# Kernel tuning notes

Measured on AMD Instinct MI355X. Metric: run time of the kernel, lower is better.

## Reference

```python
import jax, jax.numpy as jnp
import numpy as np

D_MODEL = 2048
N_Q_HEADS = 32
N_KV_HEADS = 8
D_HEAD = 64
D_MLP = 8192
NORM_EPS = 1e-5
INIT_RANGE = 0.02
IGNORE = -100000.0
B, S = 2, 2048


def setup_inputs() -> dict:
    key = jax.random.key(0)
    ks = jax.random.split(key, 8)
    return {
        "resid_pre": jax.random.normal(ks[0], (B, S, D_MODEL), dtype=jnp.float32),
        "W_Q": jax.random.normal(ks[1], (N_Q_HEADS, D_MODEL, D_HEAD), dtype=jnp.float32) * INIT_RANGE,
        "W_K": jax.random.normal(ks[2], (N_KV_HEADS, D_MODEL, D_HEAD), dtype=jnp.float32) * INIT_RANGE,
        "W_V": jax.random.normal(ks[3], (N_KV_HEADS, D_MODEL, D_HEAD), dtype=jnp.float32) * INIT_RANGE,
        "W_O": jax.random.normal(ks[4], (N_KV_HEADS, D_HEAD, D_MODEL), dtype=jnp.float32) * INIT_RANGE,
        "g1": jnp.ones((D_MODEL,), jnp.float32),
        "b1": jnp.zeros((D_MODEL,), jnp.float32),
        "g2": jnp.ones((D_MODEL,), jnp.float32),
        "b2": jnp.zeros((D_MODEL,), jnp.float32),
        "W_in": jax.random.normal(ks[5], (D_MODEL, D_MLP), dtype=jnp.float32) * INIT_RANGE,
        "b_in": jnp.zeros((D_MLP,), jnp.float32),
        "W_out": jax.random.normal(ks[6], (D_MLP, D_MODEL), dtype=jnp.float32) * INIT_RANGE,
        "b_out": jnp.zeros((D_MODEL,), jnp.float32),
    }


def rmsnorm(x, g, b):
    # torch.var (unbiased=False) is mean-centered variance, but x itself is
    # divided (not centered) -- faithful to the source.
    mu = jnp.mean(x, axis=-1, keepdims=True)
    var = jnp.mean(jnp.square(x - mu), axis=-1, keepdims=True)
    std = jnp.sqrt(var + NORM_EPS)
    return (x / std) * g + b


def attention(x, W_Q, W_K, W_V, W_O):
    b, s, _ = x.shape
    q = jnp.einsum('bpd,hde->bphe', x, W_Q)            # [b, s, n_q, d_head]
    k = jnp.einsum('bpd,hde->bphe', x, W_K)            # [b, s, n_kv, d_head]
    v = jnp.einsum('bpd,hde->bphe', x, W_V)            # [b, s, n_kv, d_head]
    g_size = N_Q_HEADS // N_KV_HEADS
    # rearrange '(n_kv g) d' with n_kv outer, group inner
    q = q.reshape(b, s, N_KV_HEADS, g_size, D_HEAD)
    # source einsum sums over the group dim (g not in output) -- faithful
    scores = jnp.einsum('bqkgd,bskd->bkqs', q, k) / jnp.sqrt(jnp.float32(D_HEAD))
    mask = jnp.triu(jnp.ones((s, s), dtype=bool), k=1)
    scores = jnp.where(mask, jnp.float32(IGNORE), scores)
    pattern = jax.nn.softmax(scores, axis=-1)          # [b, n_kv, q, s]
    z = jnp.einsum('bskd,bkqs->bqkd', v, pattern)      # [b, q, n_kv, d_head]
    return jnp.einsum('bqkd,kde->bqe', z, W_O)


def ffn(x, W_in, b_in, W_out, b_out):
    pre = jnp.einsum('bpd,dm->bpm', x, W_in) + b_in
    post = jax.nn.relu(pre)
    return jnp.einsum('bpm,md->bpd', post, W_out) + b_out


def reference(resid_pre, W_Q, W_K, W_V, W_O, g1, b1, g2, b2, W_in, b_in, W_out, b_out):
    resid_mid = attention(rmsnorm(resid_pre, g1, b1), W_Q, W_K, W_V, W_O) + resid_pre
    resid_post = ffn(rmsnorm(resid_mid, g2, b2), W_in, b_in, W_out, b_out) + resid_mid
    return resid_post
```

## Files before the change

kernel.cpp:

```cpp
#include <hip/hip_runtime.h>
#include <hip/hip_bf16.h>


using bf16 = __hip_bfloat16;
typedef __bf16 bf16x8_t __attribute__((ext_vector_type(8)));
typedef float  f32x4_t  __attribute__((ext_vector_type(4)));

#define D_MODEL 2048
#define SEQ     2048
#define NB      2
#define NTOK    4096
#define NKV     8
#define DHEAD   64
#define DMLP    8192
#define NQKV    1536

__device__ inline void storev(float* p, float v) { *p = v; }
__device__ inline void storev(bf16* p, float v)  { *p = __float2bfloat16(v); }

__device__ inline __bf16 tobf(float x) {
    union { __hip_bfloat16 h; __bf16 b; } u;
    u.h = __float2bfloat16(x);
    return u.b;
}

__global__ __launch_bounds__(256) void transpose_f32_bf16_kernel(
    const float* __restrict__ in, bf16* __restrict__ out, int K, int N)
{
    __shared__ float tile[32][33];
    const int n0 = blockIdx.x * 32, k0 = blockIdx.y * 32;
    const int tx = threadIdx.x & 31, ty = threadIdx.x >> 5;
    #pragma unroll
    for (int i = 0; i < 32; i += 8)
        tile[ty + i][tx] = in[(size_t)(k0 + ty + i) * N + n0 + tx];
    __syncthreads();
    #pragma unroll
    for (int i = 0; i < 32; i += 8)
        out[(size_t)(n0 + ty + i) * K + k0 + tx] = __float2bfloat16(tile[tx][ty + i]);
}

__global__ __launch_bounds__(256) void head_transpose_kernel(
    const float* __restrict__ in, bf16* __restrict__ out, int ngroup)
{
    __shared__ float tile[32][65];
    const int kv = blockIdx.y;
    const int k0 = blockIdx.x * 32;
    const int t  = threadIdx.x;
    const int e  = t & 63, kk = t >> 6;
    #pragma unroll
    for (int i = 0; i < 32; i += 4) {
        float s = 0.f;
        for (int g = 0; g < ngroup; ++g)
            s += in[((size_t)(kv * ngroup + g) * 2048 + k0 + kk + i) * 64 + e];
        tile[kk + i][e] = s;
    }
    __syncthreads();
    const int k = t & 31, ee = t >> 5;
    #pragma unroll
    for (int i = 0; i < 64; i += 8)
        out[(size_t)(kv * 64 + ee + i) * 2048 + k0 + k] = __float2bfloat16(tile[k][ee + i]);
}

__global__ __launch_bounds__(256) void rmsnorm_kernel(
    const float* __restrict__ x, const float* __restrict__ g,
    const float* __restrict__ b, bf16* __restrict__ out)
{
    const int row = blockIdx.x;
    const int t = threadIdx.x;
    const float* xr = x + (size_t)row * D_MODEL;
    float4 a0 = *reinterpret_cast<const float4*>(xr + t * 8);
    float4 a1 = *reinterpret_cast<const float4*>(xr + t * 8 + 4);
    float v[8] = {a0.x, a0.y, a0.z, a0.w, a1.x, a1.y, a1.z, a1.w};
    float sum = 0.f, sumsq = 0.f;
    #pragma unroll
    for (int j = 0; j < 8; ++j) { sum += v[j]; sumsq += v[j] * v[j]; }
    #pragma unroll
    for (int o = 1; o < 64; o <<= 1) {
        sum   += __shfl_xor(sum, o);
        sumsq += __shfl_xor(sumsq, o);
    }
    __shared__ float rs[4], rq[4];
    if ((t & 63) == 0) { rs[t >> 6] = sum; rq[t >> 6] = sumsq; }
    __syncthreads();
    sum   = rs[0] + rs[1] + rs[2] + rs[3];
    sumsq = rq[0] + rq[1] + rq[2] + rq[3];
    const float mu  = sum * (1.f / D_MODEL);
    const float var = sumsq * (1.f / D_MODEL) - mu * mu;
    const float rstd = 1.f / sqrtf(var + 1e-5f);
    const int c = t * 8;
    float4 g0 = *reinterpret_cast<const float4*>(g + c);
    float4 g1 = *reinterpret_cast<const float4*>(g + c + 4);
    float4 b0 = *reinterpret_cast<const float4*>(b + c);
    float4 b1 = *reinterpret_cast<const float4*>(b + c + 4);
    float gg[8] = {g0.x, g0.y, g0.z, g0.w, g1.x, g1.y, g1.z, g1.w};
    float bb[8] = {b0.x, b0.y, b0.z, b0.w, b1.x, b1.y, b1.z, b1.w};
    bf16* op = out + (size_t)row * D_MODEL + c;
    #pragma unroll
    for (int j = 0; j < 8; ++j) op[j] = __float2bfloat16(v[j] * rstd * gg[j] + bb[j]);
}

template<int BM, int BN, typename TC, bool BIAS, bool RELU, bool RESID>
__global__ __launch_bounds__(512, 2) void gemm_pipe_kernel(
    const bf16* __restrict__ A, const bf16* __restrict__ Bt,
    TC* __restrict__ C, const float* __restrict__ bias,
    const float* __restrict__ resid, int M, int N, int K, int nbx)
{
    constexpr int BK   = 64;
    constexpr int MREP = BM / 32;
    constexpr int NREP = BN / 64;
    constexpr int AI   = (BM * BK) / 4096;
    constexpr int BI   = (BN * BK) / 4096;
    constexpr int LD   = AI + BI;

    __shared__ __align__(16) bf16 As[2][BM * BK];
    __shared__ __align__(16) bf16 Bs[2][BN * BK];

    const int nwg = gridDim.x;
    const int swz = (blockIdx.x & 7) * (nwg >> 3) + (blockIdx.x >> 3);
    const int nby = nwg / nbx;
    const int by  = swz % nby;
    const int bx  = swz / nby;
    const int row0 = by * BM, col0 = bx * BN;

    const int t  = threadIdx.x;
    const int w  = t >> 6, ln = t & 63;
    const int wm = w >> 2, wn = w & 3;
    const int lr = ln & 15, hi = ln >> 4;

    const int srow = w * 8 + (ln >> 3);
    const int skx  = ((ln & 7) ^ (ln >> 3)) * 8;

    f32x4_t acc[MREP][NREP];
    #pragma unroll
    for (int m = 0; m < MREP; ++m)
        #pragma unroll
        for (int n = 0; n < NREP; ++n) acc[m][n] = (f32x4_t){0.f, 0.f, 0.f, 0.f};

    const int NT = K / BK;

    {
        const bf16* ga = A  + (size_t)(row0 + srow) * K + skx;
        const bf16* gb = Bt + (size_t)(col0 + srow) * K + skx;
        #pragma unroll
        for (int i = 0; i < AI; ++i)
            __builtin_amdgcn_global_load_lds(
                (const __attribute__((address_space(1))) void*)(ga + (size_t)i * 64 * K),
                (__attribute__((address_space(3))) void*)(&As[0][i * 4096 + w * 512]), 16, 0, 0);
        #pragma unroll
        for (int i = 0; i < BI; ++i)
            __builtin_amdgcn_global_load_lds(
                (const __attribute__((address_space(1))) void*)(gb + (size_t)i * 64 * K),
                (__attribute__((address_space(3))) void*)(&Bs[0][i * 4096 + w * 512]), 16, 0, 0);
    }

    for (int tt = 0; tt < NT; ++tt) {
        const int c = tt & 1;
        asm volatile("s_waitcnt lgkmcnt(0)" ::: "memory");
        __builtin_amdgcn_sched_barrier(0);
        __builtin_amdgcn_s_barrier();
        __builtin_amdgcn_sched_barrier(0);
        if (tt + 1 < NT) {
            const int d = c ^ 1;
            const int kt = (tt + 1) * BK;
            const bf16* ga = A  + (size_t)(row0 + srow) * K + kt + skx;
            const bf16* gb = Bt + (size_t)(col0 + srow) * K + kt + skx;
            #pragma unroll
            for (int i = 0; i < AI; ++i)
                __builtin_amdgcn_global_load_lds(
                    (const __attribute__((address_space(1))) void*)(ga + (size_t)i * 64 * K),
                    (__attribute__((address_space(3))) void*)(&As[d][i * 4096 + w * 512]), 16, 0, 0);
            #pragma unroll
            for (int i = 0; i < BI; ++i)
                __builtin_amdgcn_global_load_lds(
                    (const __attribute__((address_space(1))) void*)(gb + (size_t)i * 64 * K),
                    (__attribute__((address_space(3))) void*)(&Bs[d][i * 4096 + w * 512]), 16, 0, 0);
            __builtin_amdgcn_sched_barrier(0);
            if constexpr (LD == 8)      asm volatile("s_waitcnt vmcnt(8)" ::: "memory");
            else if constexpr (LD == 6) asm volatile("s_waitcnt vmcnt(6)" ::: "memory");
            else                        asm volatile("s_waitcnt vmcnt(4)" ::: "memory");
        } else {
            asm volatile("s_waitcnt vmcnt(0)" ::: "memory");
        }
        __builtin_amdgcn_sched_barrier(0);
        __builtin_amdgcn_s_barrier();
        __builtin_amdgcn_sched_barrier(0);

        #pragma unroll
        for (int kk = 0; kk < 2; ++kk) {
            bf16x8_t af[MREP], bfr[NREP];
            #pragma unroll
            for (int m = 0; m < MREP; ++m) {
                const int row = wm * (BM / 2) + m * 16 + lr;
                af[m] = *reinterpret_cast<const bf16x8_t*>(
                    &As[c][row * 64 + ((kk * 32 + hi * 8) ^ ((row & 7) << 3))]);
            }
            #pragma unroll
            for (int n = 0; n < NREP; ++n) {
                const int col = wn * (BN / 4) + n * 16 + lr;
                bfr[n] = *reinterpret_cast<const bf16x8_t*>(
                    &Bs[c][col * 64 + ((kk * 32 + hi * 8) ^ ((col & 7) << 3))]);
            }
            #pragma unroll
            for (int m = 0; m < MREP; ++m)
                #pragma unroll
                for (int n = 0; n < NREP; ++n)
                    acc[m][n] = __builtin_amdgcn_mfma_f32_16x16x32_bf16(af[m], bfr[n], acc[m][n], 0, 0, 0);
        }
    }

    #pragma unroll
    for (int m = 0; m < MREP; ++m) {
        #pragma unroll
        for (int n = 0; n < NREP; ++n) {
            const int cgl = col0 + wn * (BN / 4) + n * 16 + lr;
            #pragma unroll
            for (int j = 0; j < 4; ++j) {
                const int r = row0 + wm * (BM / 2) + m * 16 + hi * 4 + j;
                float v = acc[m][n][j];
                if constexpr (BIAS)  v += bias[cgl];
                if constexpr (RELU)  v = fmaxf(v, 0.f);
                if constexpr (RESID) v += resid[(size_t)r * N + cgl];
                storev(&C[(size_t)r * N + cgl], v);
            }
        }
    }
}

template<int BN, typename TC, bool BIAS, bool RELU, bool RESID>
__global__ __launch_bounds__(512, 2) void gemm_8ph_kernel(
    const bf16* __restrict__ A, const bf16* __restrict__ Bt,
    TC* __restrict__ C, const float* __restrict__ bias,
    const float* __restrict__ resid, int M, int N, int K, int nbx)
{
    constexpr int NREP = BN / 64;
    constexpr int NH   = NREP / 2;
    constexpr int BI   = BN / 64;

    __shared__ __align__(16) bf16 As[2][256 * 64];
    __shared__ __align__(16) bf16 Bs[2][BN * 64];

    const int nwg = gridDim.x;
    const int swz = (blockIdx.x & 7) * (nwg >> 3) + (blockIdx.x >> 3);
    const int nby = nwg / nbx;
    const int by  = swz % nby;
    const int bx  = swz / nby;
    const int row0 = by * 256, col0 = bx * BN;

    const int t  = threadIdx.x;
    const int w  = t >> 6, ln = t & 63;
    const int wm = w >> 2, wn = w & 3;
    const int lr = ln & 15, hi = ln >> 4;
    const int rx = (lr & 7) << 3;

    const int srow = w * 8 + (ln >> 3);
    const int skx  = ((ln & 7) ^ (ln >> 3)) * 8;

#define STAGE_A8(u, dbuf, kt)                                                   \
    __builtin_amdgcn_global_load_lds(                                           \
        (const __attribute__((address_space(1))) void*)(A + (size_t)(row0 + (u) * 64 + srow) * K + (kt) + skx), \
        (__attribute__((address_space(3))) void*)(&As[dbuf][(u) * 4096 + w * 512]), 16, 0, 0)
#define STAGE_B8(u, dbuf, kt)                                                   \
    __builtin_amdgcn_global_load_lds(                                           \
        (const __attribute__((address_space(1))) void*)(Bt + (size_t)(col0 + (u) * 64 + srow) * K + (kt) + skx), \
        (__attribute__((address_space(3))) void*)(&Bs[dbuf][(u) * 4096 + w * 512]), 16, 0, 0)
#define PH_BAR                                                                  \
    __builtin_amdgcn_sched_barrier(0);                                          \
    __builtin_amdgcn_s_barrier();                                               \
    __builtin_amdgcn_sched_barrier(0)
#define LGKM0                                                                   \
    asm volatile("s_waitcnt lgkmcnt(0)" ::: "memory");                          \
    __builtin_amdgcn_sched_barrier(0)

    f32x4_t acc[8][NREP];
    #pragma unroll
    for (int m = 0; m < 8; ++m)
        #pragma unroll
        for (int n = 0; n < NREP; ++n) acc[m][n] = (f32x4_t){0.f, 0.f, 0.f, 0.f};

    bf16x8_t af[4][2];
    bf16x8_t bfr[NREP][2];

    const int NT = K / 64;

    STAGE_A8(0, 0, 0); STAGE_A8(2, 0, 0);
    #pragma unroll
    for (int u = 0; u < BI; ++u) STAGE_B8(u, 0, 0);
    STAGE_A8(1, 0, 0); STAGE_A8(3, 0, 0);
    asm volatile("s_waitcnt vmcnt(2)" ::: "memory");
    PH_BAR;

    for (int tt = 0; tt < NT; ++tt) {
        const int c  = tt & 1, d = c ^ 1;
        const int kn = (tt + 1) * 64;
        const bool pf = (tt + 1 < NT);

        #pragma unroll
        for (int mq = 0; mq < 4; ++mq) {
            const int row = wm * 128 + mq * 16 + lr;
            #pragma unroll
            for (int kk = 0; kk < 2; ++kk)
                af[mq][kk] = *reinterpret_cast<const bf16x8_t*>(
                    &As[c][row * 64 + ((kk * 32 + hi * 8) ^ rx)]);
        }
        #pragma unroll
        for (int n = 0; n < NH; ++n) {
            const int col = wn * (BN / 4) + n * 16 + lr;
            #pragma unroll
            for (int kk = 0; kk < 2; ++kk)
                bfr[n][kk] = *reinterpret_cast<const bf16x8_t*>(
                    &Bs[c][col * 64 + ((kk * 32 + hi * 8) ^ rx)]);
        }
        if (pf) { STAGE_A8(0, d, kn); STAGE_A8(2, d, kn); }
        PH_BAR;
        LGKM0;
        __builtin_amdgcn_s_setprio(1);
        #pragma unroll
        for (int mq = 0; mq < 4; ++mq)
            #pragma unroll
            for (int n = 0; n < NH; ++n)
                #pragma unroll
                for (int kk = 0; kk < 2; ++kk)
                    acc[mq][n] = __builtin_amdgcn_mfma_f32_16x16x32_bf16(af[mq][kk], bfr[n][kk], acc[mq][n], 0, 0, 0);
        __builtin_amdgcn_s_setprio(0);
        PH_BAR;

        #pragma unroll
        for (int n = NH; n < NREP; ++n) {
            const int col = wn * (BN / 4) + n * 16 + lr;
            #pragma unroll
            for (int kk = 0; kk < 2; ++kk)
                bfr[n][kk] = *reinterpret_cast<const bf16x8_t*>(
                    &Bs[c][col * 64 + ((kk * 32 + hi * 8) ^ rx)]);
        }
        if (pf) { STAGE_B8(0, d, kn); STAGE_B8(1, d, kn); }
        __builtin_amdgcn_sched_barrier(0);
        if (pf) { asm volatile("s_waitcnt vmcnt(4)" ::: "memory"); }
        else    { asm volatile("s_waitcnt vmcnt(0)" ::: "memory"); }
        PH_BAR;
        LGKM0;
        __builtin_amdgcn_s_setprio(1);
        #pragma unroll
        for (int mq = 0; mq < 4; ++mq)
            #pragma unroll
            for (int n = NH; n < NREP; ++n)
                #pragma unroll
                for (int kk = 0; kk < 2; ++kk)
                    acc[mq][n] = __builtin_amdgcn_mfma_f32_16x16x32_bf16(af[mq][kk], bfr[n][kk], acc[mq][n], 0, 0, 0);
        __builtin_amdgcn_s_setprio(0);
        PH_BAR;

        #pragma unroll
        for (int mq = 0; mq < 4; ++mq) {
            const int row = wm * 128 + 64 + mq * 16 + lr;
            #pragma unroll
            for (int kk = 0; kk < 2; ++kk)
                af[mq][kk] = *reinterpret_cast<const bf16x8_t*>(
                    &As[c][row * 64 + ((kk * 32 + hi * 8) ^ rx)]);
        }
        if (pf) { if constexpr (BI == 4) { STAGE_B8(2, d, kn); STAGE_B8(3, d, kn); } }
        PH_BAR;
        LGKM0;
        __builtin_amdgcn_s_setprio(1);
        #pragma unroll
        for (int mq = 0; mq < 4; ++mq)
            #pragma unroll
            for (int n = NH; n < NREP; ++n)
                #pragma unroll
                for (int kk = 0; kk < 2; ++kk)
                    acc[4 + mq][n] = __builtin_amdgcn_mfma_f32_16x16x32_bf16(af[mq][kk], bfr[n][kk], acc[4 + mq][n], 0, 0, 0);
        __builtin_amdgcn_s_setprio(0);
        PH_BAR;

        if (pf) {
            STAGE_A8(1, d, kn); STAGE_A8(3, d, kn);
            __builtin_amdgcn_sched_barrier(0);
            asm volatile("s_waitcnt vmcnt(2)" ::: "memory");
        }
        PH_BAR;
        __builtin_amdgcn_s_setprio(1);
        #pragma unroll
        for (int mq = 0; mq < 4; ++mq)
            #pragma unroll
            for (int n = 0; n < NH; ++n)
                #pragma unroll
                for (int kk = 0; kk < 2; ++kk)
                    acc[4 + mq][n] = __builtin_amdgcn_mfma_f32_16x16x32_bf16(af[mq][kk], bfr[n][kk], acc[4 + mq][n], 0, 0, 0);
        __builtin_amdgcn_s_setprio(0);
        PH_BAR;
    }

    #pragma unroll
    for (int m = 0; m < 8; ++m) {
        #pragma unroll
        for (int n = 0; n < NREP; ++n) {
            const int cgl = col0 + wn * (BN / 4) + n * 16 + lr;
            #pragma unroll
            for (int j = 0; j < 4; ++j) {
                const int r = row0 + wm * 128 + m * 16 + hi * 4 + j;
                float v = acc[m][n][j];
                if constexpr (BIAS)  v += bias[cgl];
                if constexpr (RELU)  v = fmaxf(v, 0.f);
                if constexpr (RESID) v += resid[(size_t)r * N + cgl];
                storev(&C[(size_t)r * N + cgl], v);
            }
        }
    }
#undef STAGE_A8
#undef STAGE_B8
#undef PH_BAR
#undef LGKM0
}

#define KVBLK 64
#define LP    72

__global__ __launch_bounds__(256) void mfma_attn_kernel(
    const float* __restrict__ qkv, bf16* __restrict__ z)
{
    const int a  = blockIdx.x;
    const int kv = blockIdx.y;
    const int b  = blockIdx.z;
    const int b2 = 31 - a;
    const int t  = threadIdx.x;
    const int w  = t >> 6;
    const int ln = t & 63;
    const int lr = ln & 15;
    const int hi = ln >> 4;
    const int lk = hi * 8;

    __shared__ __align__(16) bf16 Ks[KVBLK * LP];
    __shared__ __align__(16) bf16 Vt[DHEAD * LP];
    __shared__ __align__(16) bf16 Ps[64 * LP];

    bf16x8_t qfA[2], qfB[2];
    #pragma unroll
    for (int sb = 0; sb < 2; ++sb) {
        const int qrow = (sb ? b2 : a) * 64 + w * 16 + lr;
        const float* qp = qkv + (size_t)(b * SEQ + qrow) * NQKV + kv * 64;
        #pragma unroll
        for (int kk = 0; kk < 2; ++kk) {
            float4 x0 = *reinterpret_cast<const float4*>(qp + kk * 32 + lk);
            float4 x1 = *reinterpret_cast<const float4*>(qp + kk * 32 + lk + 4);
            bf16x8_t v;
            v[0] = tobf(x0.x); v[1] = tobf(x0.y); v[2] = tobf(x0.z); v[3] = tobf(x0.w);
            v[4] = tobf(x1.x); v[5] = tobf(x1.y); v[6] = tobf(x1.z); v[7] = tobf(x1.w);
            if (sb) qfB[kk] = v; else qfA[kk] = v;
        }
    }

    f32x4_t accA[4], accB[4];
    #pragma unroll
    for (int n = 0; n < 4; ++n) {
        accA[n] = (f32x4_t){0.f, 0.f, 0.f, 0.f};
        accB[n] = (f32x4_t){0.f, 0.f, 0.f, 0.f};
    }
    float mA[4] = {-1e30f, -1e30f, -1e30f, -1e30f}, lA[4] = {0.f, 0.f, 0.f, 0.f};
    float mB[4] = {-1e30f, -1e30f, -1e30f, -1e30f}, lB[4] = {0.f, 0.f, 0.f, 0.f};

    const int qcdA = a  * 64 + w * 16 + hi * 4;
    const int qcdB = b2 * 64 + w * 16 + hi * 4;

    auto process = [&](const bf16x8_t* qf, f32x4_t* acc_o, float* m_st,
                       float* l_st, int qcd, int k0g, bool diag) {
        f32x4_t s[4];
        #pragma unroll
        for (int n = 0; n < 4; ++n) s[n] = (f32x4_t){0.f, 0.f, 0.f, 0.f};
        #pragma unroll
        for (int kk = 0; kk < 2; ++kk) {
            #pragma unroll
            for (int n = 0; n < 4; ++n) {
                bf16x8_t kf = *reinterpret_cast<const bf16x8_t*>(&Ks[(n * 16 + lr) * LP + kk * 32 + lk]);
                s[n] = __builtin_amdgcn_mfma_f32_16x16x32_bf16(qf[kk], kf, s[n], 0, 0, 0);
            }
        }
        #pragma unroll
        for (int n = 0; n < 4; ++n) {
            const int colg = k0g + n * 16 + lr;
            #pragma unroll
            for (int j = 0; j < 4; ++j) {
                float val = s[n][j] * 0.125f;
                if (diag && colg > qcd + j) val = -1e30f;
                s[n][j] = val;
            }
        }
        float alpha[4], mnew[4];
        #pragma unroll
        for (int j = 0; j < 4; ++j) {
            float mx = fmaxf(fmaxf(s[0][j], s[1][j]), fmaxf(s[2][j], s[3][j]));
            mx = fmaxf(mx, __shfl_xor(mx, 1));
            mx = fmaxf(mx, __shfl_xor(mx, 2));
            mx = fmaxf(mx, __shfl_xor(mx, 4));
            mx = fmaxf(mx, __shfl_xor(mx, 8));
            mnew[j]  = fmaxf(m_st[j], mx);
            alpha[j] = __expf(m_st[j] - mnew[j]);
            m_st[j]  = mnew[j];
        }
        float psum[4] = {0.f, 0.f, 0.f, 0.f};
        #pragma unroll
        for (int n = 0; n < 4; ++n) {
            #pragma unroll
            for (int j = 0; j < 4; ++j) {
                float p = __expf(s[n][j] - mnew[j]);
                psum[j] += p;
                Ps[(w * 16 + hi * 4 + j) * LP + n * 16 + lr] = __float2bfloat16(p);
            }
        }
        #pragma unroll
        for (int j = 0; j < 4; ++j) {
            float ps = psum[j];
            ps += __shfl_xor(ps, 1);
            ps += __shfl_xor(ps, 2);
            ps += __shfl_xor(ps, 4);
            ps += __shfl_xor(ps, 8);
            l_st[j] = l_st[j] * alpha[j] + ps;
        }
        #pragma unroll
        for (int n = 0; n < 4; ++n)
            #pragma unroll
            for (int j = 0; j < 4; ++j)
                acc_o[n][j] *= alpha[j];
        #pragma unroll
        for (int kk = 0; kk < 2; ++kk) {
            bf16x8_t pa = *reinterpret_cast<const bf16x8_t*>(&Ps[(w * 16 + lr) * LP + kk * 32 + lk]);
            #pragma unroll
            for (int n = 0; n < 4; ++n) {
                bf16x8_t vf = *reinterpret_cast<const bf16x8_t*>(&Vt[(n * 16 + lr) * LP + kk * 32 + lk]);
                acc_o[n] = __builtin_amdgcn_mfma_f32_16x16x32_bf16(pa, vf, acc_o[n], 0, 0, 0);
            }
        }
    };

    for (int kt = 0; kt <= b2; ++kt) {
        const int k0g = kt * KVBLK;
        __syncthreads();
        {
            const int r   = t >> 2;
            const int c16 = (t & 3) * 16;
            const float* kb = qkv + (size_t)(b * SEQ + k0g + r) * NQKV + 512 + kv * 64 + c16;
            #pragma unroll
            for (int h = 0; h < 2; ++h) {
                float4 k0 = *reinterpret_cast<const float4*>(kb + h * 8);
                float4 k1 = *reinterpret_cast<const float4*>(kb + h * 8 + 4);
                bf16x8_t kvv;
                kvv[0] = tobf(k0.x); kvv[1] = tobf(k0.y); kvv[2] = tobf(k0.z); kvv[3] = tobf(k0.w);
                kvv[4] = tobf(k1.x); kvv[5] = tobf(k1.y); kvv[6] = tobf(k1.z); kvv[7] = tobf(k1.w);
                *reinterpret_cast<bf16x8_t*>(&Ks[r * LP + c16 + h * 8]) = kvv;
            }
        }
        {
            const int dv = w * 16;
            const float* vb = qkv + (size_t)(b * SEQ + k0g + ln) * NQKV + 1024 + kv * 64 + dv;
            #pragma unroll
            for (int h = 0; h < 4; ++h) {
                float4 v4 = *reinterpret_cast<const float4*>(vb + h * 4);
                Vt[(dv + h * 4 + 0) * LP + ln] = __float2bfloat16(v4.x);
                Vt[(dv + h * 4 + 1) * LP + ln] = __float2bfloat16(v4.y);
                Vt[(dv + h * 4 + 2) * LP + ln] = __float2bfloat16(v4.z);
                Vt[(dv + h * 4 + 3) * LP + ln] = __float2bfloat16(v4.w);
            }
        }
        __syncthreads();

        if (kt <= a) process(qfA, accA, mA, lA, qcdA, k0g, kt == a);
        process(qfB, accB, mB, lB, qcdB, k0g, kt == b2);
    }

    #pragma unroll
    for (int j = 0; j < 4; ++j) {
        const float invA = 1.f / lA[j];
        bf16* zpA = z + (size_t)(b * SEQ + qcdA + j) * (NKV * DHEAD) + kv * 64;
        const float invB = 1.f / lB[j];
        bf16* zpB = z + (size_t)(b * SEQ + qcdB + j) * (NKV * DHEAD) + kv * 64;
        #pragma unroll
        for (int n = 0; n < 4; ++n) {
            zpA[n * 16 + lr] = __float2bfloat16(accA[n][j] * invA);
            zpB[n * 16 + lr] = __float2bfloat16(accB[n][j] * invB);
        }
    }
}

extern "C" void kernel_launch(void* const* d_in, const int* in_sizes, int n_in,
                              void* d_out, int out_size, void* d_ws, size_t ws_size,
                              hipStream_t stream)
{
    const float* resid_pre = (const float*)d_in[0];
    const float* W_Q   = (const float*)d_in[1];
    const float* W_K   = (const float*)d_in[2];
    const float* W_V   = (const float*)d_in[3];
    const float* W_O   = (const float*)d_in[4];
    const float* g1    = (const float*)d_in[5];
    const float* b1    = (const float*)d_in[6];
    const float* g2    = (const float*)d_in[7];
    const float* b2    = (const float*)d_in[8];
    const float* W_in  = (const float*)d_in[9];
    const float* b_in  = (const float*)d_in[10];
    const float* W_out = (const float*)d_in[11];
    const float* b_out = (const float*)d_in[12];
    float* out = (float*)d_out;

    char* ws = (char*)d_ws;
    const size_t OFF_WBIG  = 0;
    const size_t OFF_WOT   = OFF_WBIG + (size_t)DMLP * D_MODEL * 2;
    const size_t OFF_X1    = OFF_WOT  + (size_t)D_MODEL * 512 * 2;
    const size_t OFF_RMID  = OFF_X1   + (size_t)NTOK * D_MODEL * 2;
    const size_t OFF_POST  = OFF_RMID + (size_t)NTOK * D_MODEL * 4;
    const size_t OFF_WQKVT = OFF_POST;
    const size_t OFF_QKV   = OFF_WQKVT + (size_t)NQKV * D_MODEL * 2;
    const size_t OFF_Z     = OFF_QKV   + (size_t)NTOK * NQKV * 4;

    bf16*  winT   = (bf16*) (ws + OFF_WBIG);
    bf16*  woutT  = (bf16*) (ws + OFF_WBIG);
    bf16*  woT    = (bf16*) (ws + OFF_WOT);
    bf16*  x1     = (bf16*) (ws + OFF_X1);
    float* rmid   = (float*)(ws + OFF_RMID);
    bf16*  post   = (bf16*) (ws + OFF_POST);
    bf16*  wqkvT  = (bf16*) (ws + OFF_WQKVT);
    float* qkv    = (float*)(ws + OFF_QKV);
    bf16*  zbuf   = (bf16*) (ws + OFF_Z);

    transpose_f32_bf16_kernel<<<dim3(DMLP / 32, D_MODEL / 32), 256, 0, stream>>>(W_in, winT, D_MODEL, DMLP);
    head_transpose_kernel<<<dim3(D_MODEL / 32, NKV), 256, 0, stream>>>(W_Q, wqkvT, 4);
    head_transpose_kernel<<<dim3(D_MODEL / 32, NKV), 256, 0, stream>>>(W_K, wqkvT + (size_t)512  * D_MODEL, 1);
    head_transpose_kernel<<<dim3(D_MODEL / 32, NKV), 256, 0, stream>>>(W_V, wqkvT + (size_t)1024 * D_MODEL, 1);
    transpose_f32_bf16_kernel<<<dim3(D_MODEL / 32, 512 / 32), 256, 0, stream>>>(W_O, woT, 512, D_MODEL);

    rmsnorm_kernel<<<NTOK, 256, 0, stream>>>(resid_pre, g1, b1, x1);
    gemm_pipe_kernel<128, 128, float, false, false, false><<<384, 512, 0, stream>>>(
        x1, wqkvT, qkv, nullptr, nullptr, NTOK, NQKV, D_MODEL, NQKV / 128);
    mfma_attn_kernel<<<dim3(16, NKV, NB), 256, 0, stream>>>(qkv, zbuf);
    gemm_pipe_kernel<128, 128, float, false, false, true><<<512, 512, 0, stream>>>(
        zbuf, woT, rmid, nullptr, resid_pre, NTOK, D_MODEL, 512, D_MODEL / 128);
    rmsnorm_kernel<<<NTOK, 256, 0, stream>>>(rmid, g2, b2, x1);
    gemm_8ph_kernel<256, bf16, true, true, false><<<512, 512, 0, stream>>>(
        x1, winT, post, b_in, nullptr, NTOK, DMLP, D_MODEL, DMLP / 256);
    transpose_f32_bf16_kernel<<<dim3(D_MODEL / 32, DMLP / 32), 256, 0, stream>>>(W_out, woutT, DMLP, D_MODEL);
    gemm_8ph_kernel<128, float, true, false, true><<<256, 512, 0, stream>>>(
        post, woutT, out, b_out, rmid, NTOK, D_MODEL, DMLP, D_MODEL / 128);
}
```

Before: 535.5 us.

## Store QKV in bf16 and switch the W_out GEMM to 128x128 tiles

The QKV projection now writes bf16 instead of fp32. The attention kernel loads Q, K and V directly as bf16 vectors, which halves the QKV traffic and removes the per-element conversions. The final FFN down-projection moves from the 256x128 8-phase kernel with 256 blocks to the 128x128 pipelined kernel with 512 blocks, giving more blocks for the 256 CUs. The 8-phase kernel is specialized to BN=256, and the qcdB indexing is rewritten as an explicit formula.

```diff
diff --git a/kernel.cpp b/kernel.cpp
--- a/kernel.cpp
+++ b/kernel.cpp
@@ -18,10 +18,10 @@
 __device__ inline void storev(float* p, float v) { *p = v; }
 __device__ inline void storev(bf16* p, float v)  { *p = __float2bfloat16(v); }
 
-__device__ inline __bf16 tobf(float x) {
-    union { __hip_bfloat16 h; __bf16 b; } u;
-    u.h = __float2bfloat16(x);
-    return u.b;
+__device__ inline bf16 h_from_b(__bf16 x) {
+    union { __bf16 b; bf16 h; } u;
+    u.b = x;
+    return u.h;
 }
 
 __global__ __launch_bounds__(256) void transpose_f32_bf16_kernel(
@@ -226,25 +226,21 @@
     }
 }
 
-template<int BN, typename TC, bool BIAS, bool RELU, bool RESID>
+template<typename TC, bool BIAS, bool RELU, bool RESID>
 __global__ __launch_bounds__(512, 2) void gemm_8ph_kernel(
     const bf16* __restrict__ A, const bf16* __restrict__ Bt,
     TC* __restrict__ C, const float* __restrict__ bias,
     const float* __restrict__ resid, int M, int N, int K, int nbx)
 {
-    constexpr int NREP = BN / 64;
-    constexpr int NH   = NREP / 2;
-    constexpr int BI   = BN / 64;
-
     __shared__ __align__(16) bf16 As[2][256 * 64];
-    __shared__ __align__(16) bf16 Bs[2][BN * 64];
+    __shared__ __align__(16) bf16 Bs[2][256 * 64];
 
     const int nwg = gridDim.x;
     const int swz = (blockIdx.x & 7) * (nwg >> 3) + (blockIdx.x >> 3);
     const int nby = nwg / nbx;
     const int by  = swz % nby;
     const int bx  = swz / nby;
-    const int row0 = by * 256, col0 = bx * BN;
+    const int row0 = by * 256, col0 = bx * 256;
 
     const int t  = threadIdx.x;
     const int w  = t >> 6, ln = t & 63;
@@ -271,20 +267,19 @@
     asm volatile("s_waitcnt lgkmcnt(0)" ::: "memory");                          \
     __builtin_amdgcn_sched_barrier(0)
 
-    f32x4_t acc[8][NREP];
+    f32x4_t acc[8][4];
     #pragma unroll
     for (int m = 0; m < 8; ++m)
         #pragma unroll
-        for (int n = 0; n < NREP; ++n) acc[m][n] = (f32x4_t){0.f, 0.f, 0.f, 0.f};
+        for (int n = 0; n < 4; ++n) acc[m][n] = (f32x4_t){0.f, 0.f, 0.f, 0.f};
 
     bf16x8_t af[4][2];
-    bf16x8_t bfr[NREP][2];
+    bf16x8_t bfr[4][2];
 
     const int NT = K / 64;
 
     STAGE_A8(0, 0, 0); STAGE_A8(2, 0, 0);
-    #pragma unroll
-    for (int u = 0; u < BI; ++u) STAGE_B8(u, 0, 0);
+    STAGE_B8(0, 0, 0); STAGE_B8(1, 0, 0); STAGE_B8(2, 0, 0); STAGE_B8(3, 0, 0);
     STAGE_A8(1, 0, 0); STAGE_A8(3, 0, 0);
     asm volatile("s_waitcnt vmcnt(2)" ::: "memory");
     PH_BAR;
@@ -303,8 +298,8 @@
                     &As[c][row * 64 + ((kk * 32 + hi * 8) ^ rx)]);
         }
         #pragma unroll
-        for (int n = 0; n < NH; ++n) {
-            const int col = wn * (BN / 4) + n * 16 + lr;
+        for (int n = 0; n < 2; ++n) {
+            const int col = wn * 64 + n * 16 + lr;
             #pragma unroll
             for (int kk = 0; kk < 2; ++kk)
                 bfr[n][kk] = *reinterpret_cast<const bf16x8_t*>(
@@ -317,7 +312,7 @@
         #pragma unroll
         for (int mq = 0; mq < 4; ++mq)
             #pragma unroll
-            for (int n = 0; n < NH; ++n)
+            for (int n = 0; n < 2; ++n)
                 #pragma unroll
                 for (int kk = 0; kk < 2; ++kk)
                     acc[mq][n] = __builtin_amdgcn_mfma_f32_16x16x32_bf16(af[mq][kk], bfr[n][kk], acc[mq][n], 0, 0, 0);
@@ -325,8 +320,8 @@
         PH_BAR;
 
         #pragma unroll
-        for (int n = NH; n < NREP; ++n) {
-            const int col = wn * (BN / 4) + n * 16 + lr;
+        for (int n = 2; n < 4; ++n) {
+            const int col = wn * 64 + n * 16 + lr;
             #pragma unroll
             for (int kk = 0; kk < 2; ++kk)
                 bfr[n][kk] = *reinterpret_cast<const bf16x8_t*>(
@@ -342,7 +337,7 @@
         #pragma unroll
         for (int mq = 0; mq < 4; ++mq)
             #pragma unroll
-            for (int n = NH; n < NREP; ++n)
+            for (int n = 2; n < 4; ++n)
                 #pragma unroll
                 for (int kk = 0; kk < 2; ++kk)
                     acc[mq][n] = __builtin_amdgcn_mfma_f32_16x16x32_bf16(af[mq][kk], bfr[n][kk], acc[mq][n], 0, 0, 0);
@@ -357,14 +352,14 @@
                 af[mq][kk] = *reinterpret_cast<const bf16x8_t*>(
                     &As[c][row * 64 + ((kk * 32 + hi * 8) ^ rx)]);
         }
-        if (pf) { if constexpr (BI == 4) { STAGE_B8(2, d, kn); STAGE_B8(3, d, kn); } }
+        if (pf) { STAGE_B8(2, d, kn); STAGE_B8(3, d, kn); }
         PH_BAR;
         LGKM0;
         __builtin_amdgcn_s_setprio(1);
         #pragma unroll
         for (int mq = 0; mq < 4; ++mq)
             #pragma unroll
-            for (int n = NH; n < NREP; ++n)
+            for (int n = 2; n < 4; ++n)
                 #pragma unroll
                 for (int kk = 0; kk < 2; ++kk)
                     acc[4 + mq][n] = __builtin_amdgcn_mfma_f32_16x16x32_bf16(af[mq][kk], bfr[n][kk], acc[4 + mq][n], 0, 0, 0);
@@ -381,7 +376,7 @@
         #pragma unroll
         for (int mq = 0; mq < 4; ++mq)
             #pragma unroll
-            for (int n = 0; n < NH; ++n)
+            for (int n = 0; n < 2; ++n)
                 #pragma unroll
                 for (int kk = 0; kk < 2; ++kk)
                     acc[4 + mq][n] = __builtin_amdgcn_mfma_f32_16x16x32_bf16(af[mq][kk], bfr[n][kk], acc[4 + mq][n], 0, 0, 0);
@@ -392,8 +387,8 @@
     #pragma unroll
     for (int m = 0; m < 8; ++m) {
         #pragma unroll
-        for (int n = 0; n < NREP; ++n) {
-            const int cgl = col0 + wn * (BN / 4) + n * 16 + lr;
+        for (int n = 0; n < 4; ++n) {
+            const int cgl = col0 + wn * 64 + n * 16 + lr;
             #pragma unroll
             for (int j = 0; j < 4; ++j) {
                 const int r = row0 + wm * 128 + m * 16 + hi * 4 + j;
@@ -415,7 +410,7 @@
 #define LP    72
 
 __global__ __launch_bounds__(256) void mfma_attn_kernel(
-    const float* __restrict__ qkv, bf16* __restrict__ z)
+    const bf16* __restrict__ qkv, bf16* __restrict__ z)
 {
     const int a  = blockIdx.x;
     const int kv = blockIdx.y;
@@ -436,14 +431,10 @@
     #pragma unroll
     for (int sb = 0; sb < 2; ++sb) {
         const int qrow = (sb ? b2 : a) * 64 + w * 16 + lr;
-        const float* qp = qkv + (size_t)(b * SEQ + qrow) * NQKV + kv * 64;
+        const bf16* qp = qkv + (size_t)(b * SEQ + qrow) * NQKV + kv * 64;
         #pragma unroll
         for (int kk = 0; kk < 2; ++kk) {
-            float4 x0 = *reinterpret_cast<const float4*>(qp + kk * 32 + lk);
-            float4 x1 = *reinterpret_cast<const float4*>(qp + kk * 32 + lk + 4);
-            bf16x8_t v;
-            v[0] = tobf(x0.x); v[1] = tobf(x0.y); v[2] = tobf(x0.z); v[3] = tobf(x0.w);
-            v[4] = tobf(x1.x); v[5] = tobf(x1.y); v[6] = tobf(x1.z); v[7] = tobf(x1.w);
+            bf16x8_t v = *reinterpret_cast<const bf16x8_t*>(qp + kk * 32 + lk);
             if (sb) qfB[kk] = v; else qfA[kk] = v;
         }
     }
@@ -458,7 +449,7 @@
     float mB[4] = {-1e30f, -1e30f, -1e30f, -1e30f}, lB[4] = {0.f, 0.f, 0.f, 0.f};
 
     const int qcdA = a  * 64 + w * 16 + hi * 4;
-    const int qcdB = b2 * 64 + w * 16 + hi * 4;
+    const int qcdB = 31 * 64 - a * 64 + w * 16 + hi * 4;
 
     auto process = [&](const bf16x8_t* qf, f32x4_t* acc_o, float* m_st,
                        float* l_st, int qcd, int k0g, bool diag) {
@@ -536,27 +527,19 @@
         {
             const int r   = t >> 2;
             const int c16 = (t & 3) * 16;
-            const float* kb = qkv + (size_t)(b * SEQ + k0g + r) * NQKV + 512 + kv * 64 + c16;
-            #pragma unroll
-            for (int h = 0; h < 2; ++h) {
-                float4 k0 = *reinterpret_cast<const float4*>(kb + h * 8);
-                float4 k1 = *reinterpret_cast<const float4*>(kb + h * 8 + 4);
-                bf16x8_t kvv;
-                kvv[0] = tobf(k0.x); kvv[1] = tobf(k0.y); kvv[2] = tobf(k0.z); kvv[3] = tobf(k0.w);
-                kvv[4] = tobf(k1.x); kvv[5] = tobf(k1.y); kvv[6] = tobf(k1.z); kvv[7] = tobf(k1.w);
-                *reinterpret_cast<bf16x8_t*>(&Ks[r * LP + c16 + h * 8]) = kvv;
-            }
+            const bf16* kb = qkv + (size_t)(b * SEQ + k0g + r) * NQKV + 512 + kv * 64 + c16;
+            *reinterpret_cast<bf16x8_t*>(&Ks[r * LP + c16])     = *reinterpret_cast<const bf16x8_t*>(kb);
+            *reinterpret_cast<bf16x8_t*>(&Ks[r * LP + c16 + 8]) = *reinterpret_cast<const bf16x8_t*>(kb + 8);
         }
         {
             const int dv = w * 16;
-            const float* vb = qkv + (size_t)(b * SEQ + k0g + ln) * NQKV + 1024 + kv * 64 + dv;
-            #pragma unroll
-            for (int h = 0; h < 4; ++h) {
-                float4 v4 = *reinterpret_cast<const float4*>(vb + h * 4);
-                Vt[(dv + h * 4 + 0) * LP + ln] = __float2bfloat16(v4.x);
-                Vt[(dv + h * 4 + 1) * LP + ln] = __float2bfloat16(v4.y);
-                Vt[(dv + h * 4 + 2) * LP + ln] = __float2bfloat16(v4.z);
-                Vt[(dv + h * 4 + 3) * LP + ln] = __float2bfloat16(v4.w);
+            const bf16* vb = qkv + (size_t)(b * SEQ + k0g + ln) * NQKV + 1024 + kv * 64 + dv;
+            bf16x8_t v0 = *reinterpret_cast<const bf16x8_t*>(vb);
+            bf16x8_t v1 = *reinterpret_cast<const bf16x8_t*>(vb + 8);
+            #pragma unroll
+            for (int i = 0; i < 8; ++i) {
+                Vt[(dv + i)     * LP + ln] = h_from_b(v0[i]);
+                Vt[(dv + 8 + i) * LP + ln] = h_from_b(v1[i]);
             }
         }
         __syncthreads();
@@ -606,7 +589,7 @@
     const size_t OFF_POST  = OFF_RMID + (size_t)NTOK * D_MODEL * 4;
     const size_t OFF_WQKVT = OFF_POST;
     const size_t OFF_QKV   = OFF_WQKVT + (size_t)NQKV * D_MODEL * 2;
-    const size_t OFF_Z     = OFF_QKV   + (size_t)NTOK * NQKV * 4;
+    const size_t OFF_Z     = OFF_QKV   + (size_t)NTOK * NQKV * 2;
 
     bf16*  winT   = (bf16*) (ws + OFF_WBIG);
     bf16*  woutT  = (bf16*) (ws + OFF_WBIG);
@@ -615,7 +598,7 @@
     float* rmid   = (float*)(ws + OFF_RMID);
     bf16*  post   = (bf16*) (ws + OFF_POST);
     bf16*  wqkvT  = (bf16*) (ws + OFF_WQKVT);
-    float* qkv    = (float*)(ws + OFF_QKV);
+    bf16*  qkv    = (bf16*) (ws + OFF_QKV);
     bf16*  zbuf   = (bf16*) (ws + OFF_Z);
 
     transpose_f32_bf16_kernel<<<dim3(DMLP / 32, D_MODEL / 32), 256, 0, stream>>>(W_in, winT, D_MODEL, DMLP);
@@ -625,15 +608,15 @@
     transpose_f32_bf16_kernel<<<dim3(D_MODEL / 32, 512 / 32), 256, 0, stream>>>(W_O, woT, 512, D_MODEL);
 
     rmsnorm_kernel<<<NTOK, 256, 0, stream>>>(resid_pre, g1, b1, x1);
-    gemm_pipe_kernel<128, 128, float, false, false, false><<<384, 512, 0, stream>>>(
+    gemm_pipe_kernel<128, 128, bf16, false, false, false><<<384, 512, 0, stream>>>(
         x1, wqkvT, qkv, nullptr, nullptr, NTOK, NQKV, D_MODEL, NQKV / 128);
     mfma_attn_kernel<<<dim3(16, NKV, NB), 256, 0, stream>>>(qkv, zbuf);
     gemm_pipe_kernel<128, 128, float, false, false, true><<<512, 512, 0, stream>>>(
         zbuf, woT, rmid, nullptr, resid_pre, NTOK, D_MODEL, 512, D_MODEL / 128);
     rmsnorm_kernel<<<NTOK, 256, 0, stream>>>(rmid, g2, b2, x1);
-    gemm_8ph_kernel<256, bf16, true, true, false><<<512, 512, 0, stream>>>(
+    gemm_8ph_kernel<bf16, true, true, false><<<512, 512, 0, stream>>>(
         x1, winT, post, b_in, nullptr, NTOK, DMLP, D_MODEL, DMLP / 256);
     transpose_f32_bf16_kernel<<<dim3(D_MODEL / 32, DMLP / 32), 256, 0, stream>>>(W_out, woutT, DMLP, D_MODEL);
-    gemm_8ph_kernel<128, float, true, false, true><<<256, 512, 0, stream>>>(
+    gemm_pipe_kernel<128, 128, float, true, false, true><<<512, 512, 0, stream>>>(
         post, woutT, out, b_out, rmid, NTOK, D_MODEL, DMLP, D_MODEL / 128);
 }
```

Result: faster. 495.2 us (-7.5%).
